# Optimization experiments

Hardware: AMD Instinct MI355X
Metric: run time of the kernel (lower is better)

The kernel has to match this reference:

```python
import jax, jax.numpy as jnp
import numpy as np

N, IN_FEAT, LAT_FEAT, OUT_FEAT = 131072, 128, 128, 256
NUM_EXPERTS, TOP_K, OMEGA = 8, 2, 30.0


def setup_inputs() -> dict:
    key = jax.random.key(0)
    ks = jax.random.split(key, 8)
    u = lambda k_, shape, lim: jax.random.uniform(k_, shape, jnp.float32, -lim, lim)
    w_lim = np.sqrt(6.0 / IN_FEAT) / OMEGA  # SIREN init for non-first layers
    return {
        "x": jax.random.normal(ks[0], (N, IN_FEAT), jnp.float32),
        "latents": jax.random.normal(ks[1], (N, LAT_FEAT), jnp.float32),
        "gate_w": u(ks[2], (IN_FEAT, NUM_EXPERTS), 1.0 / np.sqrt(IN_FEAT)),
        "gate_b": jnp.zeros((NUM_EXPERTS,), jnp.float32),
        "W": u(ks[3], (NUM_EXPERTS, IN_FEAT, OUT_FEAT), w_lim),
        "b": u(ks[4], (NUM_EXPERTS, OUT_FEAT), 1.0 / np.sqrt(IN_FEAT)),
        "Wl": u(ks[5], (NUM_EXPERTS, LAT_FEAT, 2 * OUT_FEAT), 1.0 / np.sqrt(LAT_FEAT)),
        "bl": u(ks[6], (NUM_EXPERTS, 2 * OUT_FEAT), 1.0 / np.sqrt(LAT_FEAT)),
    }


def reference(x, latents, gate_w, gate_b, W, b, Wl, bl):
    # Gating: top-k over expert logits, softmax over the selected k logits.
    logits = x @ gate_w + gate_b                      # [N, E]
    top_vals, top_idx = jax.lax.top_k(logits, TOP_K)  # [N, k]
    top_w = jax.nn.softmax(top_vals, axis=-1)         # [N, k]
    # Dense combine weights: combine[n, e] = sum_i top_w[n, i] * (top_idx[n,i]==e).
    # Mathematically identical to the masked gather/scatter loop in torch.
    combine = jnp.sum(
        jax.nn.one_hot(top_idx, NUM_EXPERTS, dtype=x.dtype) * top_w[..., None],
        axis=1,
    )  # [N, E]
    out = jnp.zeros((x.shape[0], OUT_FEAT), x.dtype)
    for e in range(NUM_EXPERTS):  # fixed small loop over experts
        h = x @ W[e] + b[e]                    # [N, out]
        lat = latents @ Wl[e] + bl[e]          # [N, 2*out]
        scale, shift = lat[:, :OUT_FEAT], lat[:, OUT_FEAT:]
        out = out + combine[:, e:e + 1] * jnp.sin(OMEGA * h * scale + shift)
    return (out, latents)
```

## Files before the change

kernel.cpp:

```cpp
#include <hip/hip_runtime.h>

#define INF_  128
#define OUTF  256
#define LATF  128
#define OUT2  512
#define NEXP  8
#define OMEGA_ 30.0f

typedef float  f32x4  __attribute__((ext_vector_type(4)));
typedef __bf16 bf16x8 __attribute__((ext_vector_type(8)));
typedef unsigned short ushort8 __attribute__((ext_vector_type(8)));

#define PACK_THREADS (NEXP * 4 * 4 * 3 * 4 * 64)
#define EXP_STRIDE   (4 * 4 * 3 * 4 * 512)
#define PH_STRIDE    6144
#define GEMM_COMPUTE 1056
#define COPY_BLOCKS  512
#define CAP          131072

__device__ __forceinline__ unsigned short bfbits(float f) {
    unsigned int u = __builtin_bit_cast(unsigned int, f);
    return (unsigned short)((u + 0x7FFFu + ((u >> 16) & 1u)) >> 16);
}

__device__ __forceinline__ bf16x8 cvt8(f32x4 a, f32x4 b) {
    bf16x8 r;
    r[0] = (__bf16)a.x; r[1] = (__bf16)a.y; r[2] = (__bf16)a.z; r[3] = (__bf16)a.w;
    r[4] = (__bf16)b.x; r[5] = (__bf16)b.y; r[6] = (__bf16)b.z; r[7] = (__bf16)b.w;
    return r;
}

__device__ __forceinline__ f32x4 bload(const unsigned short* p) {
    const ushort4 u = *(const ushort4*)p;
    f32x4 r;
    r.x = __builtin_bit_cast(float, (unsigned int)u.x << 16);
    r.y = __builtin_bit_cast(float, (unsigned int)u.y << 16);
    r.z = __builtin_bit_cast(float, (unsigned int)u.z << 16);
    r.w = __builtin_bit_cast(float, (unsigned int)u.w << 16);
    return r;
}

#define GLOAD_LDS16(g, l) __builtin_amdgcn_global_load_lds( \
    (const __attribute__((address_space(1))) unsigned int*)(g), \
    (__attribute__((address_space(3))) unsigned int*)(l), 16, 0, 0)

__global__ void prep_kernel(const float* __restrict__ x,
                            const float* __restrict__ gw,
                            const float* __restrict__ gb,
                            const float* __restrict__ W,
                            const float* __restrict__ Wl,
                            unsigned int* __restrict__ cur,
                            unsigned int* __restrict__ perm,
                            float2* __restrict__ wps,
                            unsigned short* __restrict__ Bpk,
                            int nGate)
{
    __shared__ float sgw[INF_ * NEXP];
    __shared__ int lc[64];
    __shared__ unsigned int lbase[64];
    const int tid = threadIdx.x;

    if ((int)blockIdx.x >= nGate) {
        const int t = ((int)blockIdx.x - nGate) * 256 + tid;
        if (t >= PACK_THREADS) return;
        const int l   = t & 63;
        const int ks  = (t >> 6) & 3;
        const int m3  = (t >> 8) % 3;
        const int g   = (t >> 8) / 3;
        const int nf  = g & 3, nc = (g >> 2) & 3, e = g >> 4;
        const int col = nc * 64 + nf * 16 + (l & 15);
        const int kb  = ks * 32 + (l >> 4) * 8;
        ushort8 o;
#pragma unroll
        for (int j = 0; j < 8; ++j) {
            float v;
            if (m3 == 0) v = W [((size_t)e * 128 + kb + j) * 256 + col];
            else         v = Wl[((size_t)e * 128 + kb + j) * 512 + col + (m3 == 2 ? 256 : 0)];
            o[j] = bfbits(v);
        }
        *(ushort8*)(Bpk + (size_t)t * 8) = o;
        return;
    }

    ((float4*)sgw)[tid] = ((const float4*)gw)[tid];
    if (tid < 64) lc[tid] = 0;
    __syncthreads();

    const int t = blockIdx.x * 256 + tid;
    float acc[8];
#pragma unroll
    for (int e = 0; e < 8; ++e) acc[e] = gb[e];
    const float4* xr = (const float4*)(x + (size_t)t * INF_);
#pragma unroll 8
    for (int i = 0; i < 32; ++i) {
        float4 v = xr[i];
#pragma unroll
        for (int j = 0; j < 4; ++j) {
            const float xk = (&v.x)[j];
            const float4 g0 = *(const float4*)&sgw[(i * 4 + j) * 8];
            const float4 g1 = *(const float4*)&sgw[(i * 4 + j) * 8 + 4];
            acc[0] += xk * g0.x; acc[1] += xk * g0.y; acc[2] += xk * g0.z; acc[3] += xk * g0.w;
            acc[4] += xk * g1.x; acc[5] += xk * g1.y; acc[6] += xk * g1.z; acc[7] += xk * g1.w;
        }
    }
    float best = -1e30f, sec = -1e30f; int bi = 0, si = 0;
#pragma unroll
    for (int e = 0; e < 8; ++e) {
        const float v = acc[e];
        if (v > best)      { sec = best; si = bi; best = v; bi = e; }
        else if (v > sec)  { sec = v; si = e; }
    }
    const float ew  = __expf(sec - best);
    const float inv = 1.0f / (1.0f + ew);
    const float wb  = inv, wsc = ew * inv;
    int emin, emax; float wmin, wmax;
    if (bi < si) { emin = bi; wmin = wb;  emax = si; wmax = wsc; }
    else         { emin = si; wmin = wsc; emax = bi; wmax = wb;  }
    const int pid = emin * 8 + emax;

    const int p = atomicAdd(&lc[pid], 1);
    __syncthreads();
    if (tid < 64) { lbase[tid] = lc[tid] ? atomicAdd(&cur[tid], (unsigned int)lc[tid]) : 0u; }
    __syncthreads();
    const size_t q = (size_t)pid * CAP + lbase[pid] + (unsigned int)p;
    perm[q] = (unsigned int)t;
    wps[q]  = make_float2(wmin, wmax);
}

__launch_bounds__(256, 3)
__global__ void moe_gemm_kernel(const float* __restrict__ x,
                                const float* __restrict__ lat,
                                const unsigned short* __restrict__ Bpk,
                                const float* __restrict__ bias,
                                const float* __restrict__ biasl,
                                const unsigned int* __restrict__ c,
                                const unsigned int* __restrict__ perm,
                                const float2* __restrict__ wps,
                                float* __restrict__ out,
                                float* __restrict__ lat_out)
{
    __shared__ __align__(16) unsigned short sB[2][2 * PH_STRIDE];
    __shared__ __align__(16) unsigned short sbias[6 * 256];

    const unsigned int dd = blockIdx.x;
    const int tid  = threadIdx.x;

    if (dd >= GEMM_COMPUTE) {
        const int cb = (int)dd - GEMM_COMPUTE;
        const f32x4* src = (const f32x4*)lat + (size_t)cb * 8192;
        f32x4*       dst = (f32x4*)lat_out   + (size_t)cb * 8192;
#pragma unroll
        for (int i = 0; i < 32; ++i) {
            f32x4 v = __builtin_nontemporal_load(&src[tid + i * 256]);
            __builtin_nontemporal_store(v, &dst[tid + i * 256]);
        }
        return;
    }

    const unsigned int bid = (dd & 7) * (GEMM_COMPUTE / 8) + (dd >> 3);
    const int lane = tid & 63;

    const unsigned int n_l  = c[lane];
    const unsigned int nt_l = (n_l + 127) >> 7;
    unsigned int ts = nt_l;
#pragma unroll
    for (int s = 1; s < 64; s <<= 1) {
        unsigned int tt = __shfl_up(ts, s);
        if (lane >= s) ts += tt;
    }
    const unsigned int texcl  = ts - nt_l;
    const unsigned int ntiles = __shfl(ts, 63);
    if (bid >= ntiles) return;
    const unsigned long long mk = __ballot(bid >= texcl);
    const int pid  = __popcll(mk) - 1;
    const int tile = (int)(bid - __shfl(texcl, pid));
    const unsigned int cn = __shfl(n_l, pid);
    const int emin = pid >> 3, emax = pid & 7;
    const int rows = min(128, (int)(cn - (unsigned int)tile * 128u));
    const unsigned int* permS = perm + (size_t)pid * CAP + (size_t)tile * 128u;
    const float2* wS = wps + (size_t)pid * CAP + (size_t)tile * 128u;

    const int w    = tid >> 6;
    const int lrow = lane & 15;
    const int lgrp = lane >> 4;
    const int half = tid >> 7;
    const int wh   = (tid >> 6) & 1;
    const int t7   = tid & 127;

    const int r0 = w * 32 + lrow, r1 = r0 + 16;
    const int t0 = (int)permS[min(r0, rows - 1)];
    const int t1 = (int)permS[min(r1, rows - 1)];
    const float2 w0 = wS[min(r0, rows - 1)];
    const float2 w1 = wS[min(r1, rows - 1)];
    bf16x8 ax[2][4], al[2][4];
    {
        const float* x0 = x   + (size_t)t0 * INF_;
        const float* x1 = x   + (size_t)t1 * INF_;
        const float* l0 = lat + (size_t)t0 * LATF;
        const float* l1 = lat + (size_t)t1 * LATF;
#pragma unroll
        for (int ks = 0; ks < 4; ++ks) {
            const int kb = ks * 32 + lgrp * 8;
            ax[0][ks] = cvt8(__builtin_nontemporal_load((const f32x4*)(x0 + kb)),
                             __builtin_nontemporal_load((const f32x4*)(x0 + kb + 4)));
            ax[1][ks] = cvt8(__builtin_nontemporal_load((const f32x4*)(x1 + kb)),
                             __builtin_nontemporal_load((const f32x4*)(x1 + kb + 4)));
            al[0][ks] = cvt8(__builtin_nontemporal_load((const f32x4*)(l0 + kb)),
                             __builtin_nontemporal_load((const f32x4*)(l0 + kb + 4)));
            al[1][ks] = cvt8(__builtin_nontemporal_load((const f32x4*)(l1 + kb)),
                             __builtin_nontemporal_load((const f32x4*)(l1 + kb + 4)));
        }
    }

    const unsigned short* B0 = Bpk + (size_t)emin * EXP_STRIDE;
    const unsigned short* B1 = Bpk + (size_t)emax * EXP_STRIDE;
    const unsigned short* Bh = half ? B1 : B0;

    {
        const int i4 = (tid & 63) * 4;
        const int sg = tid >> 6;
#pragma unroll
        for (int rep = 0; rep < 2; ++rep) {
            const int seg = sg + rep * 4;
            if (seg < 6) {
                const float* bsrc =
                    (seg == 0) ? bias  + emin * OUTF :
                    (seg == 1) ? bias  + emax * OUTF :
                    (seg == 2) ? biasl + emin * OUT2 :
                    (seg == 3) ? biasl + emin * OUT2 + 256 :
                    (seg == 4) ? biasl + emax * OUT2 :
                                 biasl + emax * OUT2 + 256;
                const f32x4 v = *(const f32x4*)(bsrc + i4);
                ushort4 u;
                u.x = bfbits(v.x); u.y = bfbits(v.y); u.z = bfbits(v.z); u.w = bfbits(v.w);
                *(ushort4*)&sbias[seg * 256 + i4] = u;
            }
        }
    }

    auto STAGE = [&](int ph, int buf) {
        const unsigned short* src = Bh + (size_t)ph * PH_STRIDE + (size_t)t7 * 8;
        unsigned short* dst = &sB[buf][half * PH_STRIDE + wh * 512];
#pragma unroll
        for (int r = 0; r < 6; ++r)
            GLOAD_LDS16(src + r * 1024, dst + r * 1024);
    };

    f32x4 acc[2][3][2];
    auto COMPUTE = [&](int buf) {
#pragma unroll
        for (int ex = 0; ex < 2; ++ex)
#pragma unroll
            for (int m = 0; m < 3; ++m)
#pragma unroll
                for (int mf = 0; mf < 2; ++mf) acc[ex][m][mf] = (f32x4)0.0f;
#pragma unroll
        for (int ex = 0; ex < 2; ++ex) {
#pragma unroll
            for (int m = 0; m < 3; ++m) {
                bf16x8 bb[4];
#pragma unroll
                for (int ks = 0; ks < 4; ++ks)
                    bb[ks] = *(const bf16x8*)&sB[buf][ex * PH_STRIDE + (m * 4 + ks) * 512 + lane * 8];
#pragma unroll
                for (int ks = 0; ks < 4; ++ks) {
#pragma unroll
                    for (int mf = 0; mf < 2; ++mf) {
                        const bf16x8 a = (m == 0) ? ax[mf][ks] : al[mf][ks];
                        acc[ex][m][mf] = __builtin_amdgcn_mfma_f32_16x16x32_bf16(bb[ks], a, acc[ex][m][mf], 0, 0, 0);
                    }
                }
            }
        }
    };

    auto EPILOGUE = [&](int ph, bool guard) {
        const int cb = ph * 16 + lgrp * 4;
        const f32x4 b0h = bload(&sbias[0 * 256 + cb]);
        const f32x4 b1h = bload(&sbias[1 * 256 + cb]);
        const f32x4 b0s = bload(&sbias[2 * 256 + cb]);
        const f32x4 b0f = bload(&sbias[3 * 256 + cb]);
        const f32x4 b1s = bload(&sbias[4 * 256 + cb]);
        const f32x4 b1f = bload(&sbias[5 * 256 + cb]);
#pragma unroll
        for (int mf = 0; mf < 2; ++mf) {
            const int  rr  = mf ? r1 : r0;
            if (guard && rr >= rows) continue;
            const int  tok = mf ? t1 : t0;
            const float wmn = mf ? w1.x : w0.x;
            const float wmx = mf ? w1.y : w0.y;
            f32x4 v;
#pragma unroll
            for (int j = 0; j < 4; ++j) {
                const float h0 = acc[0][0][mf][j] + b0h[j];
                const float s0 = acc[0][1][mf][j] + b0s[j];
                const float f0 = acc[0][2][mf][j] + b0f[j];
                const float h1 = acc[1][0][mf][j] + b1h[j];
                const float s1 = acc[1][1][mf][j] + b1s[j];
                const float f1 = acc[1][2][mf][j] + b1f[j];
                v[j] = wmn * __sinf(OMEGA_ * h0 * s0 + f0)
                     + wmx * __sinf(OMEGA_ * h1 * s1 + f1);
            }
            __builtin_nontemporal_store(v, (f32x4*)(out + (size_t)tok * OUTF + cb));
        }
    };

    STAGE(0, 0);
    asm volatile("s_waitcnt vmcnt(0) lgkmcnt(0)" ::: "memory");
    __builtin_amdgcn_s_barrier();
    __builtin_amdgcn_sched_barrier(0);

    if (rows == 128) {
#pragma unroll 1
        for (int ph = 0; ph < 16; ++ph) {
            const int buf = ph & 1;
            if (ph < 15) STAGE(ph + 1, buf ^ 1);
            COMPUTE(buf);
            EPILOGUE(ph, false);
            __builtin_amdgcn_sched_barrier(0);
            if (ph < 15) {
                asm volatile("s_waitcnt vmcnt(2)" ::: "memory");
                __builtin_amdgcn_s_barrier();
                __builtin_amdgcn_sched_barrier(0);
            }
        }
    } else {
#pragma unroll 1
        for (int ph = 0; ph < 16; ++ph) {
            const int buf = ph & 1;
            if (ph > 0) {
                STAGE(ph, buf);
                asm volatile("s_waitcnt vmcnt(0)" ::: "memory");
                __builtin_amdgcn_s_barrier();
                __builtin_amdgcn_sched_barrier(0);
            }
            COMPUTE(buf);
            EPILOGUE(ph, true);
            __builtin_amdgcn_s_barrier();
            __builtin_amdgcn_sched_barrier(0);
        }
    }
}

extern "C" void kernel_launch(void* const* d_in, const int* in_sizes, int n_in,
                              void* d_out, int out_size, void* d_ws, size_t ws_size,
                              hipStream_t stream)
{
    const float* x   = (const float*)d_in[0];
    const float* lat = (const float*)d_in[1];
    const float* gw  = (const float*)d_in[2];
    const float* gb  = (const float*)d_in[3];
    const float* W   = (const float*)d_in[4];
    const float* b   = (const float*)d_in[5];
    const float* Wl  = (const float*)d_in[6];
    const float* bl  = (const float*)d_in[7];
    float* out = (float*)d_out;
    const int N = in_sizes[0] / INF_;

    char* ws = (char*)d_ws;
    unsigned int*   cur  = (unsigned int*)ws;
    unsigned short* Bpk  = (unsigned short*)(ws + 4096);
    unsigned int*   perm = (unsigned int*)(ws + (4096 + 2 * (size_t)EXP_STRIDE * NEXP + 4096));
    float2*         wps  = (float2*)((char*)perm + (size_t)64 * CAP * sizeof(unsigned int));

    (void)hipMemsetAsync(cur, 0, 256, stream);

    const int nGate = N / 256;
    prep_kernel<<<dim3(nGate + PACK_THREADS / 256), 256, 0, stream>>>(
        x, gw, gb, W, Wl, cur, perm, wps, Bpk, nGate);

    moe_gemm_kernel<<<dim3(GEMM_COMPUTE + COPY_BLOCKS), 256, 0, stream>>>(
        x, lat, Bpk, b, bl, cur, perm, wps, out, out + (size_t)N * OUTF);
}
```

Baseline: 155.7 us.

## Fold latents copy into GEMM blocks and defer epilogue stores by one phase

Removes the separate copy blocks that forwarded `latents` to the output. Each of the first 1024 GEMM tiles now copies one 64 KB chunk, one f32x4 per thread per phase, interleaved with the MFMA phases. The epilogue is also split into a compute step and a store step, so each phase's output stores are issued during the next phase. The `s_waitcnt` counts are adjusted to account for the extra in-flight memory ops. This should hide the copy and store traffic behind compute, at the cost of more live registers and more complex wait accounting.

```diff
diff --git a/kernel.cpp b/kernel.cpp
--- a/kernel.cpp
+++ b/kernel.cpp
@@ -15,8 +15,9 @@
 #define EXP_STRIDE   (4 * 4 * 3 * 4 * 512)
 #define PH_STRIDE    6144
 #define GEMM_COMPUTE 1056
-#define COPY_BLOCKS  512
 #define CAP          131072
+
+template<bool B> struct BoolC { static constexpr bool value = B; };
 
 __device__ __forceinline__ unsigned short bfbits(float f) {
     unsigned int u = __builtin_bit_cast(unsigned int, f);
@@ -144,19 +145,6 @@
 
     const unsigned int dd = blockIdx.x;
     const int tid  = threadIdx.x;
-
-    if (dd >= GEMM_COMPUTE) {
-        const int cb = (int)dd - GEMM_COMPUTE;
-        const f32x4* src = (const f32x4*)lat + (size_t)cb * 8192;
-        f32x4*       dst = (f32x4*)lat_out   + (size_t)cb * 8192;
-#pragma unroll
-        for (int i = 0; i < 32; ++i) {
-            f32x4 v = __builtin_nontemporal_load(&src[tid + i * 256]);
-            __builtin_nontemporal_store(v, &dst[tid + i * 256]);
-        }
-        return;
-    }
-
     const unsigned int bid = (dd & 7) * (GEMM_COMPUTE / 8) + (dd >> 3);
     const int lane = tid & 63;
 
@@ -186,6 +174,11 @@
     const int half = tid >> 7;
     const int wh   = (tid >> 6) & 1;
     const int t7   = tid & 127;
+
+    const bool docp = bid < 1024u;
+    const f32x4* cps = (const f32x4*)lat     + ((size_t)bid << 12) + tid;
+    f32x4*       cpd = (f32x4*)lat_out       + ((size_t)bid << 12) + tid;
+    f32x4 cpv;
 
     const int r0 = w * 32 + lrow, r1 = r0 + 16;
     const int t0 = (int)permS[min(r0, rows - 1)];
@@ -274,7 +267,8 @@
         }
     };
 
-    auto EPILOGUE = [&](int ph, bool guard) {
+    f32x4 vsave[2];
+    auto EPI_CALC = [&](int ph) {
         const int cb = ph * 16 + lgrp * 4;
         const f32x4 b0h = bload(&sbias[0 * 256 + cb]);
         const f32x4 b1h = bload(&sbias[1 * 256 + cb]);
@@ -284,9 +278,6 @@
         const f32x4 b1f = bload(&sbias[5 * 256 + cb]);
 #pragma unroll
         for (int mf = 0; mf < 2; ++mf) {
-            const int  rr  = mf ? r1 : r0;
-            if (guard && rr >= rows) continue;
-            const int  tok = mf ? t1 : t0;
             const float wmn = mf ? w1.x : w0.x;
             const float wmx = mf ? w1.y : w0.y;
             f32x4 v;
@@ -301,7 +292,16 @@
                 v[j] = wmn * __sinf(OMEGA_ * h0 * s0 + f0)
                      + wmx * __sinf(OMEGA_ * h1 * s1 + f1);
             }
-            __builtin_nontemporal_store(v, (f32x4*)(out + (size_t)tok * OUTF + cb));
+            vsave[mf] = v;
+        }
+    };
+    auto EPI_STORE = [&](int ph, bool guard) {
+        const int cb = ph * 16 + lgrp * 4;
+#pragma unroll
+        for (int mf = 0; mf < 2; ++mf) {
+            if (guard && ((mf ? r1 : r0) >= rows)) continue;
+            __builtin_nontemporal_store(vsave[mf],
+                (f32x4*)(out + (size_t)(mf ? t1 : t0) * OUTF + cb));
         }
     };
 
@@ -311,19 +311,39 @@
     __builtin_amdgcn_sched_barrier(0);
 
     if (rows == 128) {
+        auto fastloop = [&](auto DC) {
+            constexpr bool CP = decltype(DC)::value;
 #pragma unroll 1
-        for (int ph = 0; ph < 16; ++ph) {
-            const int buf = ph & 1;
-            if (ph < 15) STAGE(ph + 1, buf ^ 1);
-            COMPUTE(buf);
-            EPILOGUE(ph, false);
-            __builtin_amdgcn_sched_barrier(0);
-            if (ph < 15) {
-                asm volatile("s_waitcnt vmcnt(2)" ::: "memory");
-                __builtin_amdgcn_s_barrier();
+            for (int ph = 0; ph < 16; ++ph) {
+                const int buf = ph & 1;
+                if (ph < 15) STAGE(ph + 1, buf ^ 1);
                 __builtin_amdgcn_sched_barrier(0);
-            }
-        }
+                if constexpr (CP) {
+                    if (ph > 0) __builtin_nontemporal_store(cpv, cpd + (ph - 1) * 256);
+                    cpv = __builtin_nontemporal_load(cps + ph * 256);
+                }
+                if (ph > 0) EPI_STORE(ph - 1, false);
+                __builtin_amdgcn_sched_barrier(0);
+                COMPUTE(buf);
+                EPI_CALC(ph);
+                __builtin_amdgcn_sched_barrier(0);
+                if (ph < 15) {
+                    if (ph == 0) {
+                        if constexpr (CP) asm volatile("s_waitcnt vmcnt(1)" ::: "memory");
+                        else              asm volatile("s_waitcnt vmcnt(0)" ::: "memory");
+                    } else {
+                        if constexpr (CP) asm volatile("s_waitcnt vmcnt(4)" ::: "memory");
+                        else              asm volatile("s_waitcnt vmcnt(2)" ::: "memory");
+                    }
+                    __builtin_amdgcn_s_barrier();
+                    __builtin_amdgcn_sched_barrier(0);
+                }
+            }
+            if constexpr (CP) __builtin_nontemporal_store(cpv, cpd + 15 * 256);
+            EPI_STORE(15, false);
+        };
+        if (docp) fastloop(BoolC<true>{});
+        else      fastloop(BoolC<false>{});
     } else {
 #pragma unroll 1
         for (int ph = 0; ph < 16; ++ph) {
@@ -334,11 +354,17 @@
                 __builtin_amdgcn_s_barrier();
                 __builtin_amdgcn_sched_barrier(0);
             }
+            if (docp) {
+                if (ph > 0) __builtin_nontemporal_store(cpv, cpd + (ph - 1) * 256);
+                cpv = __builtin_nontemporal_load(cps + ph * 256);
+            }
             COMPUTE(buf);
-            EPILOGUE(ph, true);
+            EPI_CALC(ph);
+            EPI_STORE(ph, true);
             __builtin_amdgcn_s_barrier();
             __builtin_amdgcn_sched_barrier(0);
         }
+        if (docp) __builtin_nontemporal_store(cpv, cpd + 15 * 256);
     }
 }
 
@@ -369,6 +395,6 @@
     prep_kernel<<<dim3(nGate + PACK_THREADS / 256), 256, 0, stream>>>(
         x, gw, gb, W, Wl, cur, perm, wps, Bpk, nGate);
 
-    moe_gemm_kernel<<<dim3(GEMM_COMPUTE + COPY_BLOCKS), 256, 0, stream>>>(
+    moe_gemm_kernel<<<dim3(GEMM_COMPUTE), 256, 0, stream>>>(
         x, lat, Bpk, b, bl, cur, perm, wps, out, out + (size_t)N * OUTF);
 }
```

After: 189.2 us. 1.22x slower.

## Load expert weight fragments directly into registers instead of LDS staging

Applied to the files above, without the earlier changes.

Removes the double-buffered LDS staging of packed expert weights and the barriers that went with it. Each wave now loads B fragments straight from global memory (L2-resident) into a three-slot register ring, prefetching the next group while issuing MFMAs on the current one. Bias is folded into the accumulator initialisation, and the separate full and partial tile paths are merged into one guarded loop. Launch bounds drop to two blocks per CU to make room for the extra registers. This risks more global and L2 traffic, since every wave now fetches its own copy of the weights, and lower occupancy.

```diff
diff --git a/kernel.cpp b/kernel.cpp
--- a/kernel.cpp
+++ b/kernel.cpp
@@ -16,6 +16,7 @@
 #define PH_STRIDE    6144
 #define GEMM_COMPUTE 1056
 #define COPY_BLOCKS  512
+#define GEMM_GRID    (GEMM_COMPUTE + COPY_BLOCKS)
 #define CAP          131072
 
 __device__ __forceinline__ unsigned short bfbits(float f) {
@@ -39,10 +40,6 @@
     r.w = __builtin_bit_cast(float, (unsigned int)u.w << 16);
     return r;
 }
-
-#define GLOAD_LDS16(g, l) __builtin_amdgcn_global_load_lds( \
-    (const __attribute__((address_space(1))) unsigned int*)(g), \
-    (__attribute__((address_space(3))) unsigned int*)(l), 16, 0, 0)
 
 __global__ void prep_kernel(const float* __restrict__ x,
                             const float* __restrict__ gw,
@@ -127,7 +124,7 @@
     wps[q]  = make_float2(wmin, wmax);
 }
 
-__launch_bounds__(256, 3)
+__launch_bounds__(256, 2)
 __global__ void moe_gemm_kernel(const float* __restrict__ x,
                                 const float* __restrict__ lat,
                                 const unsigned short* __restrict__ Bpk,
@@ -139,7 +136,6 @@
                                 float* __restrict__ out,
                                 float* __restrict__ lat_out)
 {
-    __shared__ __align__(16) unsigned short sB[2][2 * PH_STRIDE];
     __shared__ __align__(16) unsigned short sbias[6 * 256];
 
     const unsigned int dd = blockIdx.x;
@@ -183,9 +179,6 @@
     const int w    = tid >> 6;
     const int lrow = lane & 15;
     const int lgrp = lane >> 4;
-    const int half = tid >> 7;
-    const int wh   = (tid >> 6) & 1;
-    const int t7   = tid & 127;
 
     const int r0 = w * 32 + lrow, r1 = r0 + 16;
     const int t0 = (int)permS[min(r0, rows - 1)];
@@ -211,10 +204,6 @@
                              __builtin_nontemporal_load((const f32x4*)(l1 + kb + 4)));
         }
     }
-
-    const unsigned short* B0 = Bpk + (size_t)emin * EXP_STRIDE;
-    const unsigned short* B1 = Bpk + (size_t)emax * EXP_STRIDE;
-    const unsigned short* Bh = half ? B1 : B0;
 
     {
         const int i4 = (tid & 63) * 4;
@@ -237,107 +226,80 @@
             }
         }
     }
-
-    auto STAGE = [&](int ph, int buf) {
-        const unsigned short* src = Bh + (size_t)ph * PH_STRIDE + (size_t)t7 * 8;
-        unsigned short* dst = &sB[buf][half * PH_STRIDE + wh * 512];
-#pragma unroll
-        for (int r = 0; r < 6; ++r)
-            GLOAD_LDS16(src + r * 1024, dst + r * 1024);
+    asm volatile("s_waitcnt lgkmcnt(0)" ::: "memory");
+    __builtin_amdgcn_s_barrier();
+
+    const unsigned short* Bb0 = Bpk + (size_t)emin * EXP_STRIDE + lane * 8;
+    const unsigned short* Bb1 = Bpk + (size_t)emax * EXP_STRIDE + lane * 8;
+
+    bf16x8 bfr[3][4];
+    f32x4  acc[2][3][2];
+
+    auto LOADG = [&](int ph, int g, int slot) {
+        const unsigned short* base = (g >= 3 ? Bb1 : Bb0)
+                                   + (size_t)ph * PH_STRIDE + (g % 3) * 2048;
+#pragma unroll
+        for (int ks = 0; ks < 4; ++ks)
+            bfr[slot][ks] = *(const bf16x8*)(base + ks * 512);
     };
-
-    f32x4 acc[2][3][2];
-    auto COMPUTE = [&](int buf) {
-#pragma unroll
-        for (int ex = 0; ex < 2; ++ex)
-#pragma unroll
-            for (int m = 0; m < 3; ++m)
-#pragma unroll
-                for (int mf = 0; mf < 2; ++mf) acc[ex][m][mf] = (f32x4)0.0f;
-#pragma unroll
-        for (int ex = 0; ex < 2; ++ex) {
-#pragma unroll
-            for (int m = 0; m < 3; ++m) {
-                bf16x8 bb[4];
-#pragma unroll
-                for (int ks = 0; ks < 4; ++ks)
-                    bb[ks] = *(const bf16x8*)&sB[buf][ex * PH_STRIDE + (m * 4 + ks) * 512 + lane * 8];
-#pragma unroll
-                for (int ks = 0; ks < 4; ++ks) {
-#pragma unroll
-                    for (int mf = 0; mf < 2; ++mf) {
-                        const bf16x8 a = (m == 0) ? ax[mf][ks] : al[mf][ks];
-                        acc[ex][m][mf] = __builtin_amdgcn_mfma_f32_16x16x32_bf16(bb[ks], a, acc[ex][m][mf], 0, 0, 0);
-                    }
+    auto MMAG = [&](int g) {
+        const int ex = g / 3, m = g % 3;
+#pragma unroll
+        for (int ks = 0; ks < 4; ++ks)
+#pragma unroll
+            for (int mf = 0; mf < 2; ++mf) {
+                const bf16x8 a = (m == 0) ? ax[mf][ks] : al[mf][ks];
+                acc[ex][m][mf] = __builtin_amdgcn_mfma_f32_16x16x32_bf16(
+                                     bfr[g % 3][ks], a, acc[ex][m][mf], 0, 0, 0);
+            }
+    };
+
+    LOADG(0, 0, 0);
+    LOADG(0, 1, 1);
+
+#pragma unroll 1
+    for (int ph = 0; ph < 16; ++ph) {
+        const int cb = ph * 16 + lgrp * 4;
+        {
+            const f32x4 b0h = bload(&sbias[0 * 256 + cb]);
+            const f32x4 b1h = bload(&sbias[1 * 256 + cb]);
+            const f32x4 b0s = bload(&sbias[2 * 256 + cb]);
+            const f32x4 b0f = bload(&sbias[3 * 256 + cb]);
+            const f32x4 b1s = bload(&sbias[4 * 256 + cb]);
+            const f32x4 b1f = bload(&sbias[5 * 256 + cb]);
+#pragma unroll
+            for (int mf = 0; mf < 2; ++mf) {
+                acc[0][0][mf] = b0h; acc[0][1][mf] = b0s; acc[0][2][mf] = b0f;
+                acc[1][0][mf] = b1h; acc[1][1][mf] = b1s; acc[1][2][mf] = b1f;
+            }
+        }
+#pragma unroll
+        for (int g = 0; g < 6; ++g) {
+            if (g < 4)        LOADG(ph, g + 2, (g + 2) % 3);
+            else if (ph < 15) LOADG(ph + 1, g - 4, (g - 4) % 3);
+            MMAG(g);
+        }
+#pragma unroll
+        for (int mf = 0; mf < 2; ++mf) {
+            const int rr = mf ? r1 : r0;
+            if (rr < rows) {
+                const float wmn = mf ? w1.x : w0.x;
+                const float wmx = mf ? w1.y : w0.y;
+                f32x4 v;
+#pragma unroll
+                for (int j = 0; j < 4; ++j) {
+                    const float h0 = acc[0][0][mf][j];
+                    const float s0 = acc[0][1][mf][j];
+                    const float f0 = acc[0][2][mf][j];
+                    const float h1 = acc[1][0][mf][j];
+                    const float s1 = acc[1][1][mf][j];
+                    const float f1 = acc[1][2][mf][j];
+                    v[j] = wmn * __sinf(OMEGA_ * h0 * s0 + f0)
+                         + wmx * __sinf(OMEGA_ * h1 * s1 + f1);
                 }
+                __builtin_nontemporal_store(v,
+                    (f32x4*)(out + (size_t)(mf ? t1 : t0) * OUTF + cb));
             }
-        }
-    };
-
-    auto EPILOGUE = [&](int ph, bool guard) {
-        const int cb = ph * 16 + lgrp * 4;
-        const f32x4 b0h = bload(&sbias[0 * 256 + cb]);
-        const f32x4 b1h = bload(&sbias[1 * 256 + cb]);
-        const f32x4 b0s = bload(&sbias[2 * 256 + cb]);
-        const f32x4 b0f = bload(&sbias[3 * 256 + cb]);
-        const f32x4 b1s = bload(&sbias[4 * 256 + cb]);
-        const f32x4 b1f = bload(&sbias[5 * 256 + cb]);
-#pragma unroll
-        for (int mf = 0; mf < 2; ++mf) {
-            const int  rr  = mf ? r1 : r0;
-            if (guard && rr >= rows) continue;
-            const int  tok = mf ? t1 : t0;
-            const float wmn = mf ? w1.x : w0.x;
-            const float wmx = mf ? w1.y : w0.y;
-            f32x4 v;
-#pragma unroll
-            for (int j = 0; j < 4; ++j) {
-                const float h0 = acc[0][0][mf][j] + b0h[j];
-                const float s0 = acc[0][1][mf][j] + b0s[j];
-                const float f0 = acc[0][2][mf][j] + b0f[j];
-                const float h1 = acc[1][0][mf][j] + b1h[j];
-                const float s1 = acc[1][1][mf][j] + b1s[j];
-                const float f1 = acc[1][2][mf][j] + b1f[j];
-                v[j] = wmn * __sinf(OMEGA_ * h0 * s0 + f0)
-                     + wmx * __sinf(OMEGA_ * h1 * s1 + f1);
-            }
-            __builtin_nontemporal_store(v, (f32x4*)(out + (size_t)tok * OUTF + cb));
-        }
-    };
-
-    STAGE(0, 0);
-    asm volatile("s_waitcnt vmcnt(0) lgkmcnt(0)" ::: "memory");
-    __builtin_amdgcn_s_barrier();
-    __builtin_amdgcn_sched_barrier(0);
-
-    if (rows == 128) {
-#pragma unroll 1
-        for (int ph = 0; ph < 16; ++ph) {
-            const int buf = ph & 1;
-            if (ph < 15) STAGE(ph + 1, buf ^ 1);
-            COMPUTE(buf);
-            EPILOGUE(ph, false);
-            __builtin_amdgcn_sched_barrier(0);
-            if (ph < 15) {
-                asm volatile("s_waitcnt vmcnt(2)" ::: "memory");
-                __builtin_amdgcn_s_barrier();
-                __builtin_amdgcn_sched_barrier(0);
-            }
-        }
-    } else {
-#pragma unroll 1
-        for (int ph = 0; ph < 16; ++ph) {
-            const int buf = ph & 1;
-            if (ph > 0) {
-                STAGE(ph, buf);
-                asm volatile("s_waitcnt vmcnt(0)" ::: "memory");
-                __builtin_amdgcn_s_barrier();
-                __builtin_amdgcn_sched_barrier(0);
-            }
-            COMPUTE(buf);
-            EPILOGUE(ph, true);
-            __builtin_amdgcn_s_barrier();
-            __builtin_amdgcn_sched_barrier(0);
         }
     }
 }
@@ -369,6 +331,6 @@
     prep_kernel<<<dim3(nGate + PACK_THREADS / 256), 256, 0, stream>>>(
         x, gw, gb, W, Wl, cur, perm, wps, Bpk, nGate);
 
-    moe_gemm_kernel<<<dim3(GEMM_COMPUTE + COPY_BLOCKS), 256, 0, stream>>>(
+    moe_gemm_kernel<<<dim3(GEMM_GRID), 256, 0, stream>>>(
         x, lat, Bpk, b, bl, cur, perm, wps, out, out + (size_t)N * OUTF);
 }
```

Measured after the change: 161.1 us. 1.03x slower.
